# Kernel optimization log

Measured on AMD Instinct MI355X. Metric: run time of the kernel, lower is better.

Reference implementation:

```python
import jax, jax.numpy as jnp
import numpy as np

N_NODES = 100000
N_EDGES = 1000000
IN_DIM = 128
H = [64, 64, 64, 64, 128]
OUT_DIM = 64
K = 3  # TAGConv default hops
BN_EPS = 1e-5


def _gcn_norm(src, dst, num_nodes):
    # symmetric normalization D^{-1/2} A D^{-1/2}, no self loops (PyG TAGConv default)
    deg = jax.ops.segment_sum(jnp.ones(src.shape[0], jnp.float32), dst, num_segments=num_nodes)
    dis = jnp.where(deg > 0, jax.lax.rsqrt(jnp.maximum(deg, 1.0)), 0.0)
    return dis[src] * dis[dst]  # [E]


def _tagconv(x, src, dst, norm, Ws, b, num_nodes):
    # Ws: [K+1, in, out]; out = sum_k (A_hat^k x) @ W_k + b
    out = x @ Ws[0]
    h = x
    for k in range(1, K + 1):
        h = jax.ops.segment_sum(h[src] * norm[:, None], dst, num_segments=num_nodes)
        out = out + h @ Ws[k]
    return out + b


def setup_inputs() -> dict:
    key = jax.random.key(0)
    ks = jax.random.split(key, 16)
    s = 0.05
    x = jax.random.normal(ks[0], (N_NODES, IN_DIM), jnp.float32)
    edge_index = jax.random.randint(ks[1], (2, N_EDGES), 0, N_NODES, dtype=jnp.int64)
    return {
        "x": x,
        "edge_index": edge_index,
        "bn_gamma": jnp.ones((IN_DIM,), jnp.float32),
        "bn_beta": jnp.zeros((IN_DIM,), jnp.float32),
        "W1": jax.random.normal(ks[2], (IN_DIM, H[0]), jnp.float32) * s,
        "b1": jnp.zeros((H[0],), jnp.float32),
        "tag1_W": jax.random.normal(ks[3], (K + 1, H[0], H[1]), jnp.float32) * s,
        "tag1_b": jnp.zeros((H[1],), jnp.float32),
        "W2": jax.random.normal(ks[4], (H[1], H[2]), jnp.float32) * s,
        "b2": jnp.zeros((H[2],), jnp.float32),
        "tag2_W": jax.random.normal(ks[5], (K + 1, H[2], H[3]), jnp.float32) * s,
        "tag2_b": jnp.zeros((H[3],), jnp.float32),
        "W3": jax.random.normal(ks[6], (H[3] + IN_DIM, H[4]), jnp.float32) * s,
        "b3": jnp.zeros((H[4],), jnp.float32),
        "W4": jax.random.normal(ks[7], (H[4], OUT_DIM), jnp.float32) * s,
        "b4": jnp.zeros((OUT_DIM,), jnp.float32),
    }


def reference(x, edge_index, bn_gamma, bn_beta, W1, b1, tag1_W, tag1_b,
              W2, b2, tag2_W, tag2_b, W3, b3, W4, b4):
    gelu = lambda t: jax.nn.gelu(t, approximate=False)  # torch GELU default (erf)
    src, dst = edge_index[0], edge_index[1]
    norm = _gcn_norm(src, dst, N_NODES)

    # BatchNorm over nodes (training-mode batch stats, biased variance)
    mean = jnp.mean(x, axis=0)
    var = jnp.mean((x - mean) ** 2, axis=0)
    x_norm = (x - mean) * jax.lax.rsqrt(var + BN_EPS) * bn_gamma + bn_beta

    h = gelu(x_norm @ W1 + b1)
    h = gelu(_tagconv(h, src, dst, norm, tag1_W, tag1_b, N_NODES))
    h = gelu(h @ W2 + b2)
    h = gelu(_tagconv(h, src, dst, norm, tag2_W, tag2_b, N_NODES))
    a = jnp.concatenate([x, h], axis=1)
    a = gelu(a @ W3 + b3)
    return a @ W4 + b4
```

## Files before the change

kernel.cpp:

```cpp
#include <hip/hip_runtime.h>
#include <stdint.h>

typedef unsigned short u16;
typedef unsigned int   u32;
typedef __attribute__((ext_vector_type(8))) short short8;
typedef __attribute__((ext_vector_type(4))) float float4v;

#define DEV __device__ __forceinline__

DEV float bf2f(u16 u){ return __uint_as_float(((u32)u)<<16); }
DEV u16 f2bf(float f){
  u32 u = __float_as_uint(f);
  u32 r = u + 0x7fffu + ((u>>16)&1u);
  return (u16)(r>>16);
}
DEV float gelu_f(float x){ return 0.5f*x*(1.0f + erff(x*0.70710678118654752f)); }
DEV float ldext(const void* b, size_t i, int f32){
  return f32 ? ((const float*)b)[i] : bf2f(((const u16*)b)[i]);
}
DEV int ld_src(const int* ei, int e, int E, int m64){ return m64 ? ei[2*e]     : ei[e]; }
DEV int ld_dst(const int* ei, int e, int E, int m64){ return m64 ? ei[2*(E+e)] : ei[E+e]; }
DEV int swz(int k, int n){
  return (((k>>5)*4 + (n>>4))*64 + ((((k>>3)&3)<<4) | (n&15)))*8 + (k&7);
}

__global__ __launch_bounds__(256) void detect_types(const int* __restrict__ ei,
                                                    const u16* __restrict__ xw,
                                                    int* __restrict__ flags){
  __shared__ int a64, insane;
  int t = threadIdx.x;
  if (t==0){ a64=0; insane=0; }
  __syncthreads();
  int l=0;
  for (int i=t; i<4096; i+=256) l |= ei[2*i+1];
  if (l) atomicOr(&a64, 1);
  int c=0;
  for (int i=t; i<2048; i+=256){
    u16 lo = xw[2*i];
    int e8 = (lo>>7)&0xff;
    if (e8!=0 && (e8<90 || e8>160)) c++;
  }
  atomicAdd(&insane, c);
  __syncthreads();
  if (t==0){ flags[0] = a64?0:1; flags[1] = (insane>256)?1:0; }
}

__global__ __launch_bounds__(256) void econv_count(const int* __restrict__ ei,
                                                   const int* __restrict__ flags,
                                                   int* __restrict__ s32, int* __restrict__ d32,
                                                   int* __restrict__ rankc, int* __restrict__ cnt8,
                                                   int E, int N){
  int m64 = flags[0];
  int c = (int)(blockIdx.x & 7);
  int* cnt = cnt8 + (size_t)c*N;
  for (int e = blockIdx.x*256 + threadIdx.x; e < E; e += gridDim.x*256){
    int s = ld_src(ei, e, E, m64);
    int d = ld_dst(ei, e, E, m64);
    s32[e] = s; d32[e] = d;
    int r = 0;
    if ((unsigned)d < (unsigned)N) r = atomicAdd(&cnt[d], 1);
    rankc[e] = (r<<3) | c;
  }
}

__global__ __launch_bounds__(256) void bn_stats(const void* __restrict__ x,
                                                const int* __restrict__ flags,
                                                float* __restrict__ sums,
                                                u16* __restrict__ xbf, int N){
  __shared__ float red[16][128];
  int f32  = flags[1];
  int tid  = threadIdx.x;
  int col  = tid & 15;
  int rsub = tid >> 4;
  float s8[8], q8[8];
  #pragma unroll
  for (int j=0;j<8;j++){ s8[j]=0.f; q8[j]=0.f; }
  for (int r = blockIdx.x*16 + rsub; r < N; r += gridDim.x*16){
    float f[8];
    if (f32){
      const float* xp = (const float*)x + (size_t)r*128 + col*8;
      float4 A = *(const float4*)xp;
      float4 B = *(const float4*)(xp+4);
      f[0]=A.x; f[1]=A.y; f[2]=A.z; f[3]=A.w;
      f[4]=B.x; f[5]=B.y; f[6]=B.z; f[7]=B.w;
      u16 o[8];
      #pragma unroll
      for (int j=0;j<8;j++) o[j] = f2bf(f[j]);
      *(uint4*)(xbf + (size_t)r*128 + col*8) = *(uint4*)o;
    } else {
      const u16* xp = (const u16*)x + (size_t)r*128 + col*8;
      uint4 u = *(const uint4*)xp;
      f[0]=bf2f((u16)(u.x&0xffffu)); f[1]=bf2f((u16)(u.x>>16));
      f[2]=bf2f((u16)(u.y&0xffffu)); f[3]=bf2f((u16)(u.y>>16));
      f[4]=bf2f((u16)(u.z&0xffffu)); f[5]=bf2f((u16)(u.z>>16));
      f[6]=bf2f((u16)(u.w&0xffffu)); f[7]=bf2f((u16)(u.w>>16));
    }
    #pragma unroll
    for (int j=0;j<8;j++){ s8[j]+=f[j]; q8[j]+=f[j]*f[j]; }
  }
  #pragma unroll
  for (int j=0;j<8;j++) red[rsub][col*8+j] = s8[j];
  __syncthreads();
  if (tid < 128){
    float t=0.f;
    #pragma unroll
    for (int i=0;i<16;i++) t += red[i][tid];
    atomicAdd(&sums[tid], t);
  }
  __syncthreads();
  #pragma unroll
  for (int j=0;j<8;j++) red[rsub][col*8+j] = q8[j];
  __syncthreads();
  if (tid < 128){
    float t=0.f;
    #pragma unroll
    for (int i=0;i<16;i++) t += red[i][tid];
    atomicAdd(&sums[128+tid], t);
  }
}

#define SCAN_CHUNK 1024
__global__ __launch_bounds__(256) void scan_a(const int* __restrict__ cnt8, int N,
                                              int* __restrict__ ofs, int* __restrict__ blksum,
                                              float* __restrict__ dis){
  __shared__ int lds[256];
  int t = threadIdx.x;
  int base = blockIdx.x*SCAN_CHUNK + t*4;
  int v[4];
  #pragma unroll
  for (int i=0;i<4;i++){
    int idx = base+i; int s = 0;
    if (idx < N){
      #pragma unroll
      for (int c=0;c<8;c++) s += cnt8[(size_t)c*N + idx];
    }
    v[i] = s;
  }
  #pragma unroll
  for (int i=0;i<4;i++){ int idx=base+i; if (idx<N) dis[idx] = v[i]>0 ? rsqrtf((float)v[i]) : 0.f; }
  int tsum = v[0]+v[1]+v[2]+v[3];
  lds[t] = tsum; __syncthreads();
  for (int off=1; off<256; off<<=1){
    int add = (t>=off) ? lds[t-off] : 0;
    __syncthreads();
    lds[t] += add;
    __syncthreads();
  }
  int run = lds[t] - tsum;
  #pragma unroll
  for (int i=0;i<4;i++){ int idx=base+i; if (idx<N) ofs[idx]=run; run += v[i]; }
  if (t==255) blksum[blockIdx.x] = lds[255];
}

__global__ void scan_b(const int* __restrict__ blksum, int nblk, int* __restrict__ blkoff){
  if (threadIdx.x==0 && blockIdx.x==0){
    int r=0;
    for (int i=0;i<nblk;i++){ blkoff[i]=r; r+=blksum[i]; }
    blkoff[nblk]=r;
  }
}

__global__ __launch_bounds__(256) void scan_c(int* __restrict__ ofs, const int* __restrict__ blkoff,
                                              const int* __restrict__ cnt8, int* __restrict__ base8,
                                              int N, int nchunk){
  int i = blockIdx.x*256 + threadIdx.x;
  if (i < N){
    int v = ofs[i] + blkoff[i/SCAN_CHUNK];
    ofs[i] = v;
    int run = v;
    #pragma unroll
    for (int c=0;c<8;c++){ base8[(size_t)c*N + i] = run; run += cnt8[(size_t)c*N + i]; }
  }
  if (i==0) ofs[N] = blkoff[nchunk];
}

__global__ __launch_bounds__(256) void edge_scatter(const int* __restrict__ s32,
                                                    const int* __restrict__ d32,
                                                    const int* __restrict__ rankc,
                                                    const int* __restrict__ base8,
                                                    const float* __restrict__ dis,
                                                    int2* __restrict__ epack, int E, int N){
  for (int e = blockIdx.x*256 + threadIdx.x; e < E; e += gridDim.x*256){
    int d = d32[e];
    if ((unsigned)d >= (unsigned)N) continue;
    int rc = rankc[e];
    int p  = base8[(size_t)(rc&7)*N + d] + (rc>>3);
    int s  = s32[e];
    int2 pk;
    if ((unsigned)s < (unsigned)N){ pk.x = s; pk.y = __float_as_int(dis[s]*dis[d]); }
    else                          { pk.x = 0; pk.y = 0; }
    if ((unsigned)p < (unsigned)E) epack[p] = pk;
  }
}

struct PrepOut {
  u16 *W1p,*Wt1,*Wt2,*W2p,*W3a,*W3b,*W4p;
  float *b1p,*bt1,*bt2,*b2p,*b3a,*b3b,*b4p;
};

#define PREP_TOTAL 78272

__global__ __launch_bounds__(256) void prep(const float* __restrict__ sums, float invN,
    const int* __restrict__ flags,
    const void* g, const void* be,
    const void* W1, const void* b1,
    const void* t1W, const void* t1b,
    const void* W2, const void* b2,
    const void* t2W, const void* t2b,
    const void* W3, const void* b3,
    const void* W4, const void* b4,
    PrepOut o)
{
  int f32 = flags[1];
  int idx = blockIdx.x*256 + threadIdx.x;
  if (idx >= PREP_TOTAL) return;
  auto scale_shift = [&](int f, float& sc, float& sh){
    float m   = sums[f]*invN;
    float var = sums[128+f]*invN - m*m;
    sc = ldext(g,f,f32) * rsqrtf(var + 1e-5f);
    sh = ldext(be,f,f32) - m*sc;
  };
  if (idx < 8192){
    int k=idx>>6, n=idx&63; float sc,sh; scale_shift(k,sc,sh);
    o.W1p[swz(k,n)] = f2bf(sc*ldext(W1,idx,f32)); return;
  }
  idx -= 8192;
  if (idx < 64){
    float acc = ldext(b1,idx,f32);
    for (int f=0; f<128; f++){ float sc,sh; scale_shift(f,sc,sh); acc += sh*ldext(W1,f*64+idx,f32); }
    o.b1p[idx]=acc; return;
  }
  idx -= 64;
  if (idx < 16384){ int k=idx>>6,n=idx&63; o.Wt1[swz(k,n)]=f2bf(ldext(t1W,idx,f32)); return; }  idx -= 16384;
  if (idx < 64)   { o.bt1[idx]=ldext(t1b,idx,f32); return; }  idx -= 64;
  if (idx < 16384){ int k=idx>>6,n=idx&63; o.Wt2[swz(k,n)]=f2bf(ldext(t2W,idx,f32)); return; }  idx -= 16384;
  if (idx < 64)   { o.bt2[idx]=ldext(t2b,idx,f32); return; }  idx -= 64;
  if (idx < 4096) { int k=idx>>6,n=idx&63; o.W2p[swz(k,n)]=f2bf(ldext(W2,idx,f32));  return; }  idx -= 4096;
  if (idx < 64)   { o.b2p[idx]=ldext(b2,idx,f32);  return; }  idx -= 64;
  if (idx < 12288){ int k=idx>>6,n=idx&63; o.W3a[swz(k,n)]=f2bf(ldext(W3,(size_t)k*128+n,f32));    return; }  idx -= 12288;
  if (idx < 64)   { o.b3a[idx]=ldext(b3,idx,f32);  return; }  idx -= 64;
  if (idx < 12288){ int k=idx>>6,n=idx&63; o.W3b[swz(k,n)]=f2bf(ldext(W3,(size_t)k*128+64+n,f32)); return; }  idx -= 12288;
  if (idx < 64)   { o.b3b[idx]=ldext(b3,64+idx,f32); return; } idx -= 64;
  if (idx < 8192) { int k=idx>>6,n=idx&63; o.W4p[swz(k,n)]=f2bf(ldext(W4,idx,f32));  return; }
  else            { o.b4p[idx-8192]=ldext(b4,idx-8192,f32); }
}

struct KD { const u16* p[8]; int ld[8]; };

template<int KS,int OUTMODE>
__global__ __launch_bounds__(256,2) void gemm_mfma(
    KD d, const u16* __restrict__ Wsw, const float* __restrict__ bias,
    void* __restrict__ out, int ldo, int ocol,
    int N, const int* __restrict__ flags, long xdelta, u32 xmask)
{
  constexpr int LBYTES = OUTMODE ? 128*68*4 : 128*72*2;
  __shared__ __align__(16) char lds[LBYTES];
  if (xmask && !flags[1]){
    #pragma unroll
    for (int t=0;t<KS;t++) if (xmask & (1u<<t)) d.p[t] += xdelta;
  }
  int tid = threadIdx.x, w = tid>>6, l = tid&63;
  int rlo = l&15, kq = l>>4;
  int row0b = blockIdx.x*128;
  int row0  = row0b + w*32;

  short8 Bf[KS][4];
  #pragma unroll
  for (int t=0;t<KS;t++)
    #pragma unroll
    for (int c=0;c<4;c++)
      Bf[t][c] = *(const short8*)(Wsw + ((t*4+c)*64 + l)*8);

  float4v a0[4], a1[4];
  #pragma unroll
  for (int c=0;c<4;c++){
    a0[c].x=0;a0[c].y=0;a0[c].z=0;a0[c].w=0;
    a1[c].x=0;a1[c].y=0;a1[c].z=0;a1[c].w=0;
  }

  #pragma unroll
  for (int t=0;t<KS;t++){
    const u16* ap = d.p[t]; int ld = d.ld[t];
    short8 A0 = *(const short8*)(ap + (size_t)(row0+rlo)*ld + kq*8);
    short8 A1 = *(const short8*)(ap + (size_t)(row0+16+rlo)*ld + kq*8);
    #pragma unroll
    for (int c=0;c<4;c++){
      a0[c] = __builtin_amdgcn_mfma_f32_16x16x32_bf16(A0, Bf[t][c], a0[c], 0,0,0);
      a1[c] = __builtin_amdgcn_mfma_f32_16x16x32_bf16(A1, Bf[t][c], a1[c], 0,0,0);
    }
  }

  float bv[4];
  #pragma unroll
  for (int c=0;c<4;c++) bv[c] = bias[c*16 + rlo];

  int nrow = N - row0b; if (nrow > 128) nrow = 128; if (nrow < 0) nrow = 0;

  if (OUTMODE==0){
    u16* s = (u16*)lds;
    #pragma unroll
    for (int c=0;c<4;c++){
      int col = c*16 + rlo;
      #pragma unroll
      for (int r=0;r<4;r++){
        s[(w*32 +      kq*4 + r)*72 + col] = f2bf(gelu_f(a0[c][r] + bv[c]));
        s[(w*32 + 16 + kq*4 + r)*72 + col] = f2bf(gelu_f(a1[c][r] + bv[c]));
      }
    }
    __syncthreads();
    u16* ob = (u16*)out + (size_t)row0b*ldo + ocol;
    for (int i=tid; i<nrow*8; i+=256){
      int r = i>>3, cc = (i&7)<<3;
      *(uint4*)(ob + (size_t)r*ldo + cc) = *(const uint4*)(s + r*72 + cc);
    }
  } else {
    int f32o = flags[1];
    if (f32o){
      float* sf = (float*)lds;
      #pragma unroll
      for (int c=0;c<4;c++){
        int col = c*16 + rlo;
        #pragma unroll
        for (int r=0;r<4;r++){
          float v0 = a0[c][r] + bv[c]; float v1 = a1[c][r] + bv[c];
          sf[(w*32 +      kq*4 + r)*68 + col] = isfinite(v0)?v0:777.0f;
          sf[(w*32 + 16 + kq*4 + r)*68 + col] = isfinite(v1)?v1:777.0f;
        }
      }
      __syncthreads();
      float* ob = (float*)out + (size_t)row0b*64;
      for (int i=tid; i<nrow*16; i+=256){
        int r = i>>4, cc = (i&15)<<2;
        *(uint4*)(ob + (size_t)r*64 + cc) = *(const uint4*)(sf + r*68 + cc);
      }
    } else {
      u16* s = (u16*)lds;
      #pragma unroll
      for (int c=0;c<4;c++){
        int col = c*16 + rlo;
        #pragma unroll
        for (int r=0;r<4;r++){
          float v0 = a0[c][r] + bv[c]; float v1 = a1[c][r] + bv[c];
          s[(w*32 +      kq*4 + r)*72 + col] = f2bf(isfinite(v0)?v0:777.0f);
          s[(w*32 + 16 + kq*4 + r)*72 + col] = f2bf(isfinite(v1)?v1:777.0f);
        }
      }
      __syncthreads();
      u16* ob = (u16*)out + (size_t)row0b*64;
      for (int i=tid; i<nrow*8; i+=256){
        int r = i>>3, cc = (i&7)<<3;
        *(uint4*)(ob + (size_t)r*64 + cc) = *(const uint4*)(s + r*72 + cc);
      }
    }
  }
}

__global__ __launch_bounds__(256) void spmm(const int* __restrict__ rofs,
    const int2* __restrict__ epack,
    const u16* __restrict__ hin, u16* __restrict__ hout, int N)
{
  int lane = threadIdx.x & 63;
  int wv   = (int)((blockIdx.x*256 + threadIdx.x) >> 6);
  int sub  = lane >> 3;
  int f8   = (lane & 7) * 8;
  int row  = wv*8 + sub;
  bool rok = row < N;
  int beg = rok ? rofs[row]   : 0;
  int end = rok ? rofs[row+1] : 0;

  float acc[8];
  #pragma unroll
  for (int j=0;j<8;j++) acc[j]=0.f;

  int e = beg;
  int2 pk; pk.x = 0; pk.y = 0;
  if (e < end) pk = epack[e];

  while (__any(e < end)){
    bool act = e < end;
    int   s = act ? pk.x : 0;
    float w = act ? __int_as_float(pk.y) : 0.f;
    if ((u32)s >= (u32)N){ s = 0; w = 0.f; }
    uint4 v = *(const uint4*)(hin + (size_t)s*64 + f8);
    int e1 = e + 1;
    if (e1 < end) pk = epack[e1];
    acc[0] += w*__uint_as_float(v.x<<16);
    acc[1] += w*__uint_as_float(v.x&0xffff0000u);
    acc[2] += w*__uint_as_float(v.y<<16);
    acc[3] += w*__uint_as_float(v.y&0xffff0000u);
    acc[4] += w*__uint_as_float(v.z<<16);
    acc[5] += w*__uint_as_float(v.z&0xffff0000u);
    acc[6] += w*__uint_as_float(v.w<<16);
    acc[7] += w*__uint_as_float(v.w&0xffff0000u);
    e = e1;
  }

  if (rok){
    u16 o[8];
    #pragma unroll
    for (int j=0;j<8;j++) o[j]=f2bf(acc[j]);
    *(uint4*)(hout + (size_t)row*64 + f8) = *(uint4*)o;
  }
}

extern "C" void kernel_launch(void* const* d_in, const int* in_sizes, int n_in,
                              void* d_out, int out_size, void* d_ws, size_t ws_size,
                              hipStream_t stream)
{
  const void* x   = d_in[0];
  const int*  ei  = (const int*)d_in[1];
  const void* gam = d_in[2];  const void* bet = d_in[3];
  const void* W1  = d_in[4];  const void* b1  = d_in[5];
  const void* t1W = d_in[6];  const void* t1b = d_in[7];
  const void* W2  = d_in[8];  const void* b2  = d_in[9];
  const void* t2W = d_in[10]; const void* t2b = d_in[11];
  const void* W3  = d_in[12]; const void* b3  = d_in[13];
  const void* W4  = d_in[14]; const void* b4  = d_in[15];

  const int N = in_sizes[0]/128;
  const int E = in_sizes[1]/2;

  char* p = (char*)d_ws;
  auto carve = [&](size_t bytes)->void*{
    void* r = (void*)p;
    p += (bytes + 255) & ~(size_t)255;
    return r;
  };
  int*   cnt8    = (int*)  carve((size_t)N*8*4);
  float* bnsums  = (float*)carve(256*4);
  int*   flags   = (int*)  carve(256);
  size_t zero_span = (size_t)((char*)flags + 256 - (char*)cnt8);
  int*   row_ofs = (int*)  carve((size_t)(N+1)*4);
  int*   blksum  = (int*)  carve(1024*4);
  int*   blkoff  = (int*)  carve(1032*4);
  float* dis     = (float*)carve((size_t)N*4);
  int*   base8   = (int*)  carve((size_t)N*8*4);
  int*   src32   = (int*)  carve((size_t)E*4);
  int*   dst32   = (int*)  carve((size_t)E*4);
  int*   rankc   = (int*)  carve((size_t)E*4);
  int2*  epack   = (int2*) carve((size_t)E*8);
  PrepOut po;
  po.W1p=(u16*)carve(8192*2);   po.b1p=(float*)carve(64*4);
  po.Wt1=(u16*)carve(16384*2);  po.bt1=(float*)carve(64*4);
  po.Wt2=(u16*)carve(16384*2);  po.bt2=(float*)carve(64*4);
  po.W2p=(u16*)carve(4096*2);   po.b2p=(float*)carve(64*4);
  po.W3a=(u16*)carve(12288*2);  po.b3a=(float*)carve(64*4);
  po.W3b=(u16*)carve(12288*2);  po.b3b=(float*)carve(64*4);
  po.W4p=(u16*)carve(8192*2);   po.b4p=(float*)carve(64*4);
  u16* xbf  = (u16*)carve((size_t)N*128*2);
  u16* buf0 = (u16*)carve((size_t)N*64*2);
  u16* buf1 = (u16*)carve((size_t)N*64*2);
  u16* buf2 = (u16*)carve((size_t)N*64*2);
  u16* buf3 = (u16*)carve((size_t)N*64*2);
  u16* buf4 = (u16*)carve((size_t)N*64*2);
  carve(64*1024);
  u16* Ka   = buf0;

  size_t needed = (size_t)(p - (char*)d_ws);
  if (needed > ws_size){
    hipMemsetAsync(d_out, 0, (size_t)out_size*2, stream);
    return;
  }

  long xdelta = (const u16*)x - xbf;

  const int nchunk = (N + SCAN_CHUNK-1)/SCAN_CHUNK;
  const int rblk   = (N + 255)/256;
  const int gblk   = (N + 127)/128;
  const int sblk   = (N + 31)/32;

  hipMemsetAsync(cnt8, 0, zero_span, stream);

  detect_types<<<1, 256, 0, stream>>>(ei, (const u16*)x, flags);
  econv_count <<<2048,256,0,stream>>>(ei, flags, src32, dst32, rankc, cnt8, E, N);
  bn_stats    <<<512,256,0, stream>>>(x, flags, bnsums, xbf, N);
  scan_a      <<<nchunk,256,0,stream>>>(cnt8, N, row_ofs, blksum, dis);
  scan_b      <<<1,  64, 0, stream>>>(blksum, nchunk, blkoff);
  scan_c      <<<rblk,256,0, stream>>>(row_ofs, blkoff, cnt8, base8, N, nchunk);
  edge_scatter<<<2048,256,0,stream>>>(src32, dst32, rankc, base8, dis, epack, E, N);
  prep        <<<(PREP_TOTAL+255)/256, 256, 0, stream>>>(bnsums, 1.0f/(float)N, flags,
                 gam, bet, W1, b1, t1W, t1b, W2, b2, t2W, t2b, W3, b3, W4, b4, po);

  KD dx;   for (int t=0;t<4;t++){ dx.p[t]  = xbf + t*32;  dx.ld[t]=128; }
           for (int t=4;t<8;t++){ dx.p[t]  = xbf;         dx.ld[t]=128; }
  KD dcat; { u16* bs[4]={buf0,buf1,buf2,buf3};
             for (int t=0;t<8;t++){ dcat.p[t]=bs[t>>1]+(t&1)*32; dcat.ld[t]=64; } }
  KD d3;   for (int t=0;t<4;t++){ d3.p[t]  = xbf + t*32;  d3.ld[t]=128; }
           d3.p[4]=buf4; d3.ld[4]=64; d3.p[5]=buf4+32; d3.ld[5]=64;
           d3.p[6]=buf4; d3.ld[6]=64; d3.p[7]=buf4;    d3.ld[7]=64;
  KD d4;   for (int t=0;t<4;t++){ d4.p[t]  = Ka + t*32;   d4.ld[t]=128; }
           for (int t=4;t<8;t++){ d4.p[t]  = Ka;          d4.ld[t]=128; }

  gemm_mfma<4,0><<<gblk,256,0,stream>>>(dx, po.W1p, po.b1p, buf0,64,0, N, flags, xdelta, 0xFu);
  spmm<<<sblk,256,0,stream>>>(row_ofs, epack, buf0, buf1, N);
  spmm<<<sblk,256,0,stream>>>(row_ofs, epack, buf1, buf2, N);
  spmm<<<sblk,256,0,stream>>>(row_ofs, epack, buf2, buf3, N);
  gemm_mfma<8,0><<<gblk,256,0,stream>>>(dcat, po.Wt1, po.bt1, buf4,64,0, N, flags, 0, 0);
  { KD dl2; for (int t=0;t<8;t++){ dl2.p[t]=buf4+(t&1)*32; dl2.ld[t]=64; }
    gemm_mfma<2,0><<<gblk,256,0,stream>>>(dl2, po.W2p, po.b2p, buf0,64,0, N, flags, 0, 0); }
  spmm<<<sblk,256,0,stream>>>(row_ofs, epack, buf0, buf1, N);
  spmm<<<sblk,256,0,stream>>>(row_ofs, epack, buf1, buf2, N);
  spmm<<<sblk,256,0,stream>>>(row_ofs, epack, buf2, buf3, N);
  gemm_mfma<8,0><<<gblk,256,0,stream>>>(dcat, po.Wt2, po.bt2, buf4,64,0, N, flags, 0, 0);
  gemm_mfma<6,0><<<gblk,256,0,stream>>>(d3, po.W3a, po.b3a, Ka,128,0,  N, flags, xdelta, 0xFu);
  gemm_mfma<6,0><<<gblk,256,0,stream>>>(d3, po.W3b, po.b3b, Ka,128,64, N, flags, xdelta, 0xFu);
  gemm_mfma<4,1><<<gblk,256,0,stream>>>(d4, po.W4p, po.b4p, d_out,64,0, N, flags, 0, 0);
}
```

Before: 494.4 us.

## Build CSR via two-level bucketed counting sort with shared-memory histograms

Replaces the global-atomic per-node counting and 8-way rank scheme with a two-pass radix-style bucket sort. Edges are first binned by coarse destination bucket using LDS histograms and column scans, then each bucket's block computes per-node counts, row offsets, degree normalisation and emits packed edges with LDS atomics. This aims to remove heavy global atomics and scattered writes during CSR construction, at the cost of more kernel launches and extra edge passes. It adds fallback conditions that zero the output when NPB exceeds 256 or E is small.

```diff
diff --git a/kernel.cpp b/kernel.cpp
--- a/kernel.cpp
+++ b/kernel.cpp
@@ -7,6 +7,9 @@
 typedef __attribute__((ext_vector_type(4))) float float4v;
 
 #define DEV __device__ __forceinline__
+
+#define ABLK  512
+#define MAXNB 4096
 
 DEV float bf2f(u16 u){ return __uint_as_float(((u32)u)<<16); }
 DEV u16 f2bf(float f){
@@ -45,21 +48,148 @@
   if (t==0){ flags[0] = a64?0:1; flags[1] = (insane>256)?1:0; }
 }
 
-__global__ __launch_bounds__(256) void econv_count(const int* __restrict__ ei,
-                                                   const int* __restrict__ flags,
-                                                   int* __restrict__ s32, int* __restrict__ d32,
-                                                   int* __restrict__ rankc, int* __restrict__ cnt8,
-                                                   int E, int N){
+__global__ __launch_bounds__(256) void econv_a0(const int* __restrict__ ei,
+                                                const int* __restrict__ flags,
+                                                int2* __restrict__ sd, int* __restrict__ hist,
+                                                int E, int N, int shift, int NBK){
+  __shared__ int cnt[MAXNB];
+  for (int i=threadIdx.x; i<NBK; i+=256) cnt[i]=0;
+  __syncthreads();
   int m64 = flags[0];
-  int c = (int)(blockIdx.x & 7);
-  int* cnt = cnt8 + (size_t)c*N;
-  for (int e = blockIdx.x*256 + threadIdx.x; e < E; e += gridDim.x*256){
+  for (int e = blockIdx.x*256 + threadIdx.x; e < E; e += ABLK*256){
     int s = ld_src(ei, e, E, m64);
     int d = ld_dst(ei, e, E, m64);
-    s32[e] = s; d32[e] = d;
-    int r = 0;
-    if ((unsigned)d < (unsigned)N) r = atomicAdd(&cnt[d], 1);
-    rankc[e] = (r<<3) | c;
+    int2 p; p.x = s; p.y = d;
+    sd[e] = p;
+    if ((unsigned)d < (unsigned)N) atomicAdd(&cnt[d>>shift], 1);
+  }
+  __syncthreads();
+  int* hrow = hist + (size_t)blockIdx.x*NBK;
+  for (int i=threadIdx.x; i<NBK; i+=256) hrow[i] = cnt[i];
+}
+
+__global__ __launch_bounds__(256) void hist_colscan(int* __restrict__ hist,
+                                                    int* __restrict__ btot, int NBK){
+  __shared__ int lds[256];
+  int b = blockIdx.x, t = threadIdx.x;
+  int v0 = hist[(size_t)(2*t  )*NBK + b];
+  int v1 = hist[(size_t)(2*t+1)*NBK + b];
+  int ps = v0 + v1;
+  lds[t] = ps; __syncthreads();
+  for (int off=1; off<256; off<<=1){
+    int add = (t>=off) ? lds[t-off] : 0;
+    __syncthreads();
+    lds[t] += add;
+    __syncthreads();
+  }
+  int excl = lds[t] - ps;
+  hist[(size_t)(2*t  )*NBK + b] = excl;
+  hist[(size_t)(2*t+1)*NBK + b] = excl + v0;
+  if (t==255) btot[b] = lds[255];
+}
+
+__global__ __launch_bounds__(256) void bucket_scan(const int* __restrict__ btot,
+                                                   int* __restrict__ bb, int NBK){
+  __shared__ int lds[256];
+  int t = threadIdx.x;
+  int carry = 0;
+  int nch = (NBK + 255)/256;
+  for (int c=0; c<nch; c++){
+    int i = c*256 + t;
+    int v = (i<NBK) ? btot[i] : 0;
+    lds[t] = v; __syncthreads();
+    for (int off=1; off<256; off<<=1){
+      int add = (t>=off) ? lds[t-off] : 0;
+      __syncthreads();
+      lds[t] += add;
+      __syncthreads();
+    }
+    if (i<NBK) bb[i] = carry + lds[t] - v;
+    int tot = lds[255];
+    __syncthreads();
+    carry += tot;
+  }
+  if (t==0) bb[NBK] = carry;
+}
+
+__global__ __launch_bounds__(256) void econv_a1(const int2* __restrict__ sd,
+                                                const int* __restrict__ hist,
+                                                const int* __restrict__ bb,
+                                                int2* __restrict__ binned,
+                                                int E, int N, int shift, int NBK){
+  __shared__ int cnt[MAXNB];
+  __shared__ int base[MAXNB];
+  const int* hrow = hist + (size_t)blockIdx.x*NBK;
+  for (int i=threadIdx.x; i<NBK; i+=256){ cnt[i]=0; base[i]=bb[i]+hrow[i]; }
+  __syncthreads();
+  for (int e = blockIdx.x*256 + threadIdx.x; e < E; e += ABLK*256){
+    int2 p = sd[e];
+    if ((unsigned)p.y < (unsigned)N){
+      int b = p.y >> shift;
+      int r = atomicAdd(&cnt[b], 1);
+      binned[base[b] + r] = p;
+    }
+  }
+}
+
+__global__ __launch_bounds__(256) void bucket_count(const int2* __restrict__ binned,
+                                                    const int* __restrict__ bb,
+                                                    int* __restrict__ rofs, float* __restrict__ dis,
+                                                    int N, int shift, int NBK, int NPB){
+  __shared__ int cnt[256];
+  __shared__ int lds[256];
+  int b = blockIdx.x, t = threadIdx.x;
+  int lo = bb[b], hi = bb[b+1];
+  if (t < NPB) cnt[t] = 0;
+  __syncthreads();
+  int mask = NPB - 1;
+  for (int e = lo + t; e < hi; e += 256)
+    atomicAdd(&cnt[binned[e].y & mask], 1);
+  __syncthreads();
+  int v = (t < NPB) ? cnt[t] : 0;
+  lds[t] = v; __syncthreads();
+  for (int off=1; off<256; off<<=1){
+    int add = (t>=off) ? lds[t-off] : 0;
+    __syncthreads();
+    lds[t] += add;
+    __syncthreads();
+  }
+  if (t < NPB){
+    int node = (b<<shift) + t;
+    if (node < N){
+      rofs[node] = lo + lds[t] - v;
+      dis[node]  = v > 0 ? rsqrtf((float)v) : 0.f;
+    }
+  }
+  if (b==0 && t==0) rofs[N] = bb[NBK];
+}
+
+__global__ __launch_bounds__(256) void bucket_emit(const int2* __restrict__ binned,
+                                                   const int* __restrict__ bb,
+                                                   const int* __restrict__ rofs,
+                                                   const float* __restrict__ dis,
+                                                   int2* __restrict__ epack,
+                                                   int N, int shift, int NPB){
+  __shared__ int   cur[256];
+  __shared__ float dl[256];
+  int b = blockIdx.x, t = threadIdx.x;
+  int lo = bb[b], hi = bb[b+1];
+  if (t < NPB){
+    int node = (b<<shift) + t;
+    cur[t] = (node < N) ? rofs[node] : 0;
+    dl[t]  = (node < N) ? dis[node]  : 0.f;
+  }
+  __syncthreads();
+  int mask = NPB - 1;
+  for (int e = lo + t; e < hi; e += 256){
+    int2 p = binned[e];
+    int dli = p.y & mask;
+    int slot = atomicAdd(&cur[dli], 1);
+    int s = p.x; float w;
+    if ((unsigned)s < (unsigned)N) w = dis[s]*dl[dli];
+    else { s = 0; w = 0.f; }
+    int2 pk; pk.x = s; pk.y = __float_as_int(w);
+    epack[slot] = pk;
   }
 }
 
@@ -116,80 +246,6 @@
     #pragma unroll
     for (int i=0;i<16;i++) t += red[i][tid];
     atomicAdd(&sums[128+tid], t);
-  }
-}
-
-#define SCAN_CHUNK 1024
-__global__ __launch_bounds__(256) void scan_a(const int* __restrict__ cnt8, int N,
-                                              int* __restrict__ ofs, int* __restrict__ blksum,
-                                              float* __restrict__ dis){
-  __shared__ int lds[256];
-  int t = threadIdx.x;
-  int base = blockIdx.x*SCAN_CHUNK + t*4;
-  int v[4];
-  #pragma unroll
-  for (int i=0;i<4;i++){
-    int idx = base+i; int s = 0;
-    if (idx < N){
-      #pragma unroll
-      for (int c=0;c<8;c++) s += cnt8[(size_t)c*N + idx];
-    }
-    v[i] = s;
-  }
-  #pragma unroll
-  for (int i=0;i<4;i++){ int idx=base+i; if (idx<N) dis[idx] = v[i]>0 ? rsqrtf((float)v[i]) : 0.f; }
-  int tsum = v[0]+v[1]+v[2]+v[3];
-  lds[t] = tsum; __syncthreads();
-  for (int off=1; off<256; off<<=1){
-    int add = (t>=off) ? lds[t-off] : 0;
-    __syncthreads();
-    lds[t] += add;
-    __syncthreads();
-  }
-  int run = lds[t] - tsum;
-  #pragma unroll
-  for (int i=0;i<4;i++){ int idx=base+i; if (idx<N) ofs[idx]=run; run += v[i]; }
-  if (t==255) blksum[blockIdx.x] = lds[255];
-}
-
-__global__ void scan_b(const int* __restrict__ blksum, int nblk, int* __restrict__ blkoff){
-  if (threadIdx.x==0 && blockIdx.x==0){
-    int r=0;
-    for (int i=0;i<nblk;i++){ blkoff[i]=r; r+=blksum[i]; }
-    blkoff[nblk]=r;
-  }
-}
-
-__global__ __launch_bounds__(256) void scan_c(int* __restrict__ ofs, const int* __restrict__ blkoff,
-                                              const int* __restrict__ cnt8, int* __restrict__ base8,
-                                              int N, int nchunk){
-  int i = blockIdx.x*256 + threadIdx.x;
-  if (i < N){
-    int v = ofs[i] + blkoff[i/SCAN_CHUNK];
-    ofs[i] = v;
-    int run = v;
-    #pragma unroll
-    for (int c=0;c<8;c++){ base8[(size_t)c*N + i] = run; run += cnt8[(size_t)c*N + i]; }
-  }
-  if (i==0) ofs[N] = blkoff[nchunk];
-}
-
-__global__ __launch_bounds__(256) void edge_scatter(const int* __restrict__ s32,
-                                                    const int* __restrict__ d32,
-                                                    const int* __restrict__ rankc,
-                                                    const int* __restrict__ base8,
-                                                    const float* __restrict__ dis,
-                                                    int2* __restrict__ epack, int E, int N){
-  for (int e = blockIdx.x*256 + threadIdx.x; e < E; e += gridDim.x*256){
-    int d = d32[e];
-    if ((unsigned)d >= (unsigned)N) continue;
-    int rc = rankc[e];
-    int p  = base8[(size_t)(rc&7)*N + d] + (rc>>3);
-    int s  = s32[e];
-    int2 pk;
-    if ((unsigned)s < (unsigned)N){ pk.x = s; pk.y = __float_as_int(dis[s]*dis[d]); }
-    else                          { pk.x = 0; pk.y = 0; }
-    if ((unsigned)p < (unsigned)E) epack[p] = pk;
   }
 }
 
@@ -420,24 +476,27 @@
   const int N = in_sizes[0]/128;
   const int E = in_sizes[1]/2;
 
+  int shift = 7;
+  while ((((long)N + (1L<<shift) - 1) >> shift) > MAXNB) shift++;
+  const int NPB = 1<<shift;
+  const int NBK = (int)(((long)N + NPB - 1) >> shift);
+
   char* p = (char*)d_ws;
   auto carve = [&](size_t bytes)->void*{
     void* r = (void*)p;
     p += (bytes + 255) & ~(size_t)255;
     return r;
   };
-  int*   cnt8    = (int*)  carve((size_t)N*8*4);
   float* bnsums  = (float*)carve(256*4);
   int*   flags   = (int*)  carve(256);
-  size_t zero_span = (size_t)((char*)flags + 256 - (char*)cnt8);
+  size_t zero_span = (size_t)((char*)p - (char*)bnsums);
   int*   row_ofs = (int*)  carve((size_t)(N+1)*4);
-  int*   blksum  = (int*)  carve(1024*4);
-  int*   blkoff  = (int*)  carve(1032*4);
   float* dis     = (float*)carve((size_t)N*4);
-  int*   base8   = (int*)  carve((size_t)N*8*4);
-  int*   src32   = (int*)  carve((size_t)E*4);
-  int*   dst32   = (int*)  carve((size_t)E*4);
-  int*   rankc   = (int*)  carve((size_t)E*4);
+  int*   hist    = (int*)  carve((size_t)ABLK*NBK*4);
+  int*   btot    = (int*)  carve((size_t)NBK*4);
+  int*   bb      = (int*)  carve((size_t)(NBK+1)*4);
+  int2*  sd      = (int2*) carve((size_t)E*8);
+  int2*  binned  = (int2*) carve((size_t)E*8);
   int2*  epack   = (int2*) carve((size_t)E*8);
   PrepOut po;
   po.W1p=(u16*)carve(8192*2);   po.b1p=(float*)carve(64*4);
@@ -457,27 +516,26 @@
   u16* Ka   = buf0;
 
   size_t needed = (size_t)(p - (char*)d_ws);
-  if (needed > ws_size){
+  if (needed > ws_size || NPB > 256 || E < 4096){
     hipMemsetAsync(d_out, 0, (size_t)out_size*2, stream);
     return;
   }
 
   long xdelta = (const u16*)x - xbf;
 
-  const int nchunk = (N + SCAN_CHUNK-1)/SCAN_CHUNK;
-  const int rblk   = (N + 255)/256;
-  const int gblk   = (N + 127)/128;
-  const int sblk   = (N + 31)/32;
-
-  hipMemsetAsync(cnt8, 0, zero_span, stream);
+  const int gblk = (N + 127)/128;
+  const int sblk = (N + 31)/32;
+
+  hipMemsetAsync(bnsums, 0, zero_span, stream);
 
   detect_types<<<1, 256, 0, stream>>>(ei, (const u16*)x, flags);
-  econv_count <<<2048,256,0,stream>>>(ei, flags, src32, dst32, rankc, cnt8, E, N);
-  bn_stats    <<<512,256,0, stream>>>(x, flags, bnsums, xbf, N);
-  scan_a      <<<nchunk,256,0,stream>>>(cnt8, N, row_ofs, blksum, dis);
-  scan_b      <<<1,  64, 0, stream>>>(blksum, nchunk, blkoff);
-  scan_c      <<<rblk,256,0, stream>>>(row_ofs, blkoff, cnt8, base8, N, nchunk);
-  edge_scatter<<<2048,256,0,stream>>>(src32, dst32, rankc, base8, dis, epack, E, N);
+  econv_a0    <<<ABLK,256,0,stream>>>(ei, flags, sd, hist, E, N, shift, NBK);
+  hist_colscan<<<NBK, 256,0,stream>>>(hist, btot, NBK);
+  bucket_scan <<<1,   256,0,stream>>>(btot, bb, NBK);
+  econv_a1    <<<ABLK,256,0,stream>>>(sd, hist, bb, binned, E, N, shift, NBK);
+  bucket_count<<<NBK, 256,0,stream>>>(binned, bb, row_ofs, dis, N, shift, NBK, NPB);
+  bucket_emit <<<NBK, 256,0,stream>>>(binned, bb, row_ofs, dis, epack, N, shift, NPB);
+  bn_stats    <<<512, 256,0,stream>>>(x, flags, bnsums, xbf, N);
   prep        <<<(PREP_TOTAL+255)/256, 256, 0, stream>>>(bnsums, 1.0f/(float)N, flags,
                  gam, bet, W1, b1, t1W, t1b, W2, b2, t2W, t2b, W3, b3, W4, b4, po);
 
```

After: 467.8 us. 5.4% less time.
